# Performance work log

Hardware: AMD Instinct MI355X
Metric: run time of the kernel (lower is better)

## Reference

```python
import jax, jax.numpy as jnp
import numpy as np

N_NODES = 50000
N_EDGES = 800000
IN_CH = 256
OUT_CH = 64
HEADS = 4


def setup_inputs() -> dict:
    key = jax.random.key(0)
    k1, k2, k3, k4, k5 = jax.random.split(key, 5)
    x = jax.random.normal(k1, (N_NODES, IN_CH), dtype=jnp.float32)
    edge_index = jax.random.randint(k2, (2, N_EDGES), 0, N_NODES, dtype=jnp.int64)
    # xavier-ish scaled params
    weight = jax.random.normal(k3, (HEADS, IN_CH, OUT_CH), dtype=jnp.float32) * (2.0 / (IN_CH + OUT_CH)) ** 0.5
    att_src = jax.random.normal(k4, (1, HEADS, OUT_CH), dtype=jnp.float32) * 0.1
    att_dst = jax.random.normal(k5, (1, HEADS, OUT_CH), dtype=jnp.float32) * 0.1
    bias = jnp.zeros((HEADS * OUT_CH,), dtype=jnp.float32)
    return {"x": x, "edge_index": edge_index, "weight": weight,
            "att_src": att_src, "att_dst": att_dst, "bias": bias}


def reference(x, edge_index, weight, att_src, att_dst, bias):
    # GATConv forward (eval mode: dropout is identity), vectorized over heads.
    num_nodes = x.shape[0]
    row, col = edge_index[0], edge_index[1]
    # per-head projection: [N, H, C]
    x_h = jnp.einsum('nf,hfc->nhc', x, weight)
    alpha_src = jnp.sum(x_h * att_src[0], axis=-1)   # [N, H]
    alpha_dst = jnp.sum(x_h * att_dst[0], axis=-1)   # [N, H]
    alpha = alpha_src[row] + alpha_dst[col]          # [E, H]
    alpha = jax.nn.leaky_relu(alpha, negative_slope=0.2)
    # segment softmax over edges grouped by destination row (numerically stable)
    alpha_max = jax.ops.segment_max(alpha, row, num_segments=num_nodes)  # [N, H]
    alpha = jnp.exp(alpha - alpha_max[row])
    alpha_sum = jax.ops.segment_sum(alpha, row, num_segments=num_nodes)  # [N, H]
    alpha = alpha / jnp.clip(alpha_sum[row], 1e-16)
    # message passing: scatter-add alpha-weighted source features
    messages = alpha[:, :, None] * x_h[col]                              # [E, H, C]
    out = jax.ops.segment_sum(messages, row, num_segments=num_nodes)    # [N, H, C]
    out = out.reshape(num_nodes, -1) + bias                              # concat heads
    return out
```

## Files before the change

### kernel.cpp

```cpp
#include <hip/hip_runtime.h>
#include <hip/hip_fp16.h>
#include <math.h>

#define N_IN_CH 256
#define N_OUT   256
#define HEADS   4
#define OUT_CH  64
#define BM      64
#define SCAN_BLOCK 1024

typedef __attribute__((ext_vector_type(8))) short bf16x8;
typedef __attribute__((ext_vector_type(4))) float f32x4;

__device__ __forceinline__ float lrelu(float a) {
  return a >= 0.f ? a : 0.2f * a;
}

__device__ __forceinline__ ushort f2bf(float f) {
  uint u = __float_as_uint(f);
  uint r = (u + 0x7FFFu + ((u >> 16) & 1u)) >> 16;
  return (ushort)r;
}

__device__ __forceinline__ ushort f2h(float f) {
  return __half_as_ushort(__float2half(f));
}
__device__ __forceinline__ float h2f(ushort u) {
  return __half2float(__ushort_as_half(u));
}

__global__ void convert_w(const float* __restrict__ w, ushort* __restrict__ bt,
                          int* __restrict__ counts, int nnodes) {
  const int idx = blockIdx.x * 256 + threadIdx.x;
  if (idx < nnodes) counts[idx] = 0;
  const int n = idx >> 8, k = idx & 255;
  const int h = n >> 6, c = n & 63;
  bt[idx] = f2bf(w[h * (N_IN_CH * OUT_CH) + k * OUT_CH + c]);
}

__global__ void count_kernel(const int* __restrict__ row, int* __restrict__ counts,
                             int* __restrict__ rank, int nedges) {
  int e = blockIdx.x * blockDim.x + threadIdx.x;
  if (e < nedges) rank[e] = atomicAdd(&counts[row[e]], 1);
}

__global__ __launch_bounds__(256) void proj_mfma(
    const float* __restrict__ x, const ushort* __restrict__ bt,
    const float* __restrict__ att_src, const float* __restrict__ att_dst,
    ushort* __restrict__ xh, float* __restrict__ asrc, float* __restrict__ adst,
    int nnodes) {
  __shared__ ushort at[BM * N_IN_CH];
  const int tid = threadIdx.x;
  const int wave = tid >> 6;
  const int lane = tid & 63;
  const int n0 = blockIdx.x * BM;

  {
    const int rsub = tid >> 6;
    const int cf = (tid & 63) * 4;
    const int cb = cf * 2;
#pragma unroll
    for (int it = 0; it < 16; ++it) {
      const int row_ = it * 4 + rsub;
      const int grow = n0 + row_;
      float4 xv = make_float4(0.f, 0.f, 0.f, 0.f);
      if (grow < nnodes) xv = *(const float4*)&x[(size_t)grow * N_IN_CH + cf];
      ushort4 b;
      b.x = f2bf(xv.x); b.y = f2bf(xv.y); b.z = f2bf(xv.z); b.w = f2bf(xv.w);
      const int cbs = cb ^ ((row_ & 7) << 4);
      *(ushort4*)((char*)at + row_ * 512 + cbs) = b;
    }
  }
  __syncthreads();

  f32x4 acc[4][4];
#pragma unroll
  for (int mt = 0; mt < 4; ++mt)
#pragma unroll
    for (int nt = 0; nt < 4; ++nt) acc[mt][nt] = (f32x4){0.f, 0.f, 0.f, 0.f};

  const int lmod = lane & 15;
  const int ldiv = lane >> 4;

  for (int ks = 0; ks < 8; ++ks) {
    bf16x8 a[4], b[4];
#pragma unroll
    for (int mt = 0; mt < 4; ++mt) {
      const int row_ = mt * 16 + lmod;
      const int kb = ks * 64 + ldiv * 16;
      const int cbs = kb ^ ((row_ & 7) << 4);
      a[mt] = *(const bf16x8*)((const char*)at + row_ * 512 + cbs);
    }
#pragma unroll
    for (int nt = 0; nt < 4; ++nt) {
      const int n = wave * 64 + nt * 16 + lmod;
      b[nt] = *(const bf16x8*)&bt[(size_t)n * N_IN_CH + ks * 32 + ldiv * 8];
    }
#pragma unroll
    for (int mt = 0; mt < 4; ++mt)
#pragma unroll
      for (int nt = 0; nt < 4; ++nt)
        acc[mt][nt] = __builtin_amdgcn_mfma_f32_16x16x32_bf16(
            a[mt], b[nt], acc[mt][nt], 0, 0, 0);
  }

  float atts[4], attd[4];
#pragma unroll
  for (int nt = 0; nt < 4; ++nt) {
    const int gcol = wave * 64 + nt * 16 + lmod;
    atts[nt] = att_src[gcol];
    attd[nt] = att_dst[gcol];
  }

#pragma unroll
  for (int mt = 0; mt < 4; ++mt) {
#pragma unroll
    for (int reg = 0; reg < 4; ++reg) {
      const int grow = n0 + mt * 16 + ldiv * 4 + reg;
      const bool ok = grow < nnodes;
      float vs = 0.f, vd = 0.f;
#pragma unroll
      for (int nt = 0; nt < 4; ++nt) {
        const float v = acc[mt][nt][reg];
        if (ok) xh[(size_t)grow * N_OUT + wave * 64 + nt * 16 + lmod] = f2h(v);
        vs = fmaf(v, atts[nt], vs);
        vd = fmaf(v, attd[nt], vd);
      }
#pragma unroll
      for (int d = 1; d < 16; d <<= 1) {
        vs += __shfl_xor(vs, d, 64);
        vd += __shfl_xor(vd, d, 64);
      }
      if (lmod == 0 && ok) {
        asrc[grow * HEADS + wave] = vs;
        adst[grow * HEADS + wave] = vd;
      }
    }
  }
}

__global__ __launch_bounds__(SCAN_BLOCK) void scan1_kernel(
    const int* __restrict__ counts, int* __restrict__ offsets,
    int* __restrict__ partials, int n) {
  __shared__ int wsum[16];
  const int tid = threadIdx.x;
  const int lane = tid & 63;
  const int wid = tid >> 6;
  const int i = blockIdx.x * SCAN_BLOCK + tid;
  int v = (i < n) ? counts[i] : 0;
  int incl = v;
#pragma unroll
  for (int d = 1; d < 64; d <<= 1) {
    int t = __shfl_up(incl, d, 64);
    if (lane >= d) incl += t;
  }
  if (lane == 63) wsum[wid] = incl;
  __syncthreads();
  if (wid == 0) {
    int wv = (lane < 16) ? wsum[lane] : 0;
#pragma unroll
    for (int d = 1; d < 16; d <<= 1) {
      int t = __shfl_up(wv, d, 64);
      if (lane >= d) wv += t;
    }
    if (lane < 16) wsum[lane] = wv;
  }
  __syncthreads();
  const int wexcl = (wid == 0) ? 0 : wsum[wid - 1];
  if (i <= n) offsets[i] = wexcl + incl - v;
  if (tid == SCAN_BLOCK - 1) partials[blockIdx.x] = wsum[15];
}

__global__ void scan2_kernel(int* __restrict__ partials, int nparts) {
  const int lane = threadIdx.x;
  int v = (lane < nparts) ? partials[lane] : 0;
  int incl = v;
#pragma unroll
  for (int d = 1; d < 64; d <<= 1) {
    int t = __shfl_up(incl, d, 64);
    if (lane >= d) incl += t;
  }
  if (lane < nparts) partials[lane] = incl - v;
}

__global__ void scatter_kernel(const int* __restrict__ row, const int* __restrict__ col,
                               const int* __restrict__ rank,
                               const int* __restrict__ offsets,
                               const int* __restrict__ partials,
                               const float* __restrict__ asrc,
                               const float* __restrict__ adst,
                               uint4* __restrict__ erec, int nedges) {
  int e = blockIdx.x * blockDim.x + threadIdx.x;
  if (e < nedges) {
    const int r = row[e];
    const int c = col[e];
    const int pos = offsets[r] + partials[r >> 10] + rank[e];
    const float4 s = *(const float4*)&asrc[r * 4];
    const float4 d = *(const float4*)&adst[c * 4];
    uint4 rec;
    rec.x = (uint)c;
    rec.y = (uint)f2h(__expf(lrelu(s.x + d.x))) |
            ((uint)f2h(__expf(lrelu(s.y + d.y))) << 16);
    rec.z = (uint)f2h(__expf(lrelu(s.z + d.z))) |
            ((uint)f2h(__expf(lrelu(s.w + d.w))) << 16);
    rec.w = 0u;
    erec[pos] = rec;
  }
}

__global__ __launch_bounds__(256) void gather_kernel(
    const int* __restrict__ offsets, const int* __restrict__ partials,
    const uint4* __restrict__ erec,
    const ushort* __restrict__ xh, const float* __restrict__ bias,
    float* __restrict__ out, int nnodes) {
  __shared__ float pbuf[4][64 * 4];
  const int wv = threadIdx.x >> 6;
  const int lane = threadIdx.x & 63;
  const int n = blockIdx.x * 4 + wv;
  if (n >= nnodes) return;
  const int off = offsets[n] + partials[n >> 10];
  const int end = offsets[n + 1] + partials[(n + 1) >> 10];
  const int deg = end - off;
  const int half = lane >> 5;
  const int ch8 = (lane & 31) * 8;
  const int hh = (lane & 31) >> 3;

  float4 s4 = make_float4(0.f, 0.f, 0.f, 0.f);
  float a0 = 0.f, a1 = 0.f, a2 = 0.f, a3 = 0.f;
  float a4 = 0.f, a5 = 0.f, a6 = 0.f, a7 = 0.f;

  for (int b = 0; b < deg; b += 64) {
    const int cnt = min(64, deg - b);
    int cl_l = 0;
    float4 p = make_float4(0.f, 0.f, 0.f, 0.f);
    if (lane < cnt) {
      const uint4 rec = erec[off + b + lane];
      cl_l = (int)rec.x;
      p.x = h2f((ushort)(rec.y & 0xFFFFu));
      p.y = h2f((ushort)(rec.y >> 16));
      p.z = h2f((ushort)(rec.z & 0xFFFFu));
      p.w = h2f((ushort)(rec.z >> 16));
      s4.x += p.x; s4.y += p.y; s4.z += p.z; s4.w += p.w;
    }
    *(float4*)&pbuf[wv][lane * 4] = p;

    for (int j = 0; j < cnt; j += 16) {
      int cq[8];
#pragma unroll
      for (int q = 0; q < 8; ++q) cq[q] = __shfl(cl_l, j + 2 * q + half, 64);
      uint4 xq[8];
#pragma unroll
      for (int q = 0; q < 8; ++q)
        xq[q] = *(const uint4*)&xh[(size_t)cq[q] * N_OUT + ch8];

      float wq[8];
#pragma unroll
      for (int q = 0; q < 8; ++q) wq[q] = pbuf[wv][(j + 2 * q + half) * 4 + hh];

#pragma unroll
      for (int q = 0; q < 8; ++q) {
        a0 = fmaf(wq[q], h2f((ushort)(xq[q].x & 0xFFFFu)), a0);
        a1 = fmaf(wq[q], h2f((ushort)(xq[q].x >> 16)), a1);
        a2 = fmaf(wq[q], h2f((ushort)(xq[q].y & 0xFFFFu)), a2);
        a3 = fmaf(wq[q], h2f((ushort)(xq[q].y >> 16)), a3);
        a4 = fmaf(wq[q], h2f((ushort)(xq[q].z & 0xFFFFu)), a4);
        a5 = fmaf(wq[q], h2f((ushort)(xq[q].z >> 16)), a5);
        a6 = fmaf(wq[q], h2f((ushort)(xq[q].w & 0xFFFFu)), a6);
        a7 = fmaf(wq[q], h2f((ushort)(xq[q].w >> 16)), a7);
      }
    }
  }

  a0 += __shfl_xor(a0, 32, 64);
  a1 += __shfl_xor(a1, 32, 64);
  a2 += __shfl_xor(a2, 32, 64);
  a3 += __shfl_xor(a3, 32, 64);
  a4 += __shfl_xor(a4, 32, 64);
  a5 += __shfl_xor(a5, 32, 64);
  a6 += __shfl_xor(a6, 32, 64);
  a7 += __shfl_xor(a7, 32, 64);

#pragma unroll
  for (int d = 1; d < 64; d <<= 1) {
    s4.x += __shfl_xor(s4.x, d, 64);
    s4.y += __shfl_xor(s4.y, d, 64);
    s4.z += __shfl_xor(s4.z, d, 64);
    s4.w += __shfl_xor(s4.w, d, 64);
  }
  const float sh = (hh == 0) ? s4.x : (hh == 1) ? s4.y : (hh == 2) ? s4.z : s4.w;
  const float invh = 1.f / fmaxf(sh, 1e-16f);

  const int wch = ch8 + half * 4;
  const float4 b4 = *(const float4*)&bias[wch];
  float4 o;
  o.x = fmaf(half ? a4 : a0, invh, b4.x);
  o.y = fmaf(half ? a5 : a1, invh, b4.y);
  o.z = fmaf(half ? a6 : a2, invh, b4.z);
  o.w = fmaf(half ? a7 : a3, invh, b4.w);
  *(float4*)&out[(size_t)n * N_OUT + wch] = o;
}

extern "C" void kernel_launch(void* const* d_in, const int* in_sizes, int n_in,
                              void* d_out, int out_size, void* d_ws, size_t ws_size,
                              hipStream_t stream) {
  const float* x        = (const float*)d_in[0];
  const int*   edge_idx = (const int*)d_in[1];
  const float* weight   = (const float*)d_in[2];
  const float* att_src  = (const float*)d_in[3];
  const float* att_dst  = (const float*)d_in[4];
  const float* bias     = (const float*)d_in[5];
  float* out = (float*)d_out;

  const int nnodes = in_sizes[0] / N_IN_CH;
  const int nedges = in_sizes[1] / 2;
  const int* row = edge_idx;
  const int* col = edge_idx + nedges;

  char* wsb = (char*)d_ws;
  size_t woff = 0;
  auto alloc = [&](size_t bytes) -> char* {
    char* p = wsb + woff;
    woff += (bytes + 255) & ~(size_t)255;
    return p;
  };
  ushort* xh    = (ushort*)alloc((size_t)nnodes * N_OUT * sizeof(ushort));
  ushort* bt    = (ushort*)alloc((size_t)N_OUT * N_IN_CH * sizeof(ushort));
  float* asrc   = (float*)alloc((size_t)nnodes * HEADS * sizeof(float));
  float* adst   = (float*)alloc((size_t)nnodes * HEADS * sizeof(float));
  int* counts   = (int*)alloc((size_t)nnodes * sizeof(int));
  int* offsets  = (int*)alloc((size_t)(nnodes + 1) * sizeof(int));
  int* partials = (int*)alloc(256 * sizeof(int));
  int* rank     = (int*)alloc((size_t)nedges * sizeof(int));
  uint4* erec   = (uint4*)alloc((size_t)nedges * sizeof(uint4));

  convert_w<<<256, 256, 0, stream>>>(weight, bt, counts, nnodes);

  const int eblocks = (nedges + 255) / 256;
  count_kernel<<<eblocks, 256, 0, stream>>>(row, counts, rank, nedges);

  const int nblocksA = (nnodes + BM - 1) / BM;
  proj_mfma<<<nblocksA, 256, 0, stream>>>(x, bt, att_src, att_dst,
                                          xh, asrc, adst, nnodes);

  const int nscan = (nnodes + 1 + SCAN_BLOCK - 1) / SCAN_BLOCK;
  scan1_kernel<<<nscan, SCAN_BLOCK, 0, stream>>>(counts, offsets, partials, nnodes);
  scan2_kernel<<<1, 64, 0, stream>>>(partials, nscan);

  scatter_kernel<<<eblocks, 256, 0, stream>>>(row, col, rank, offsets, partials,
                                              asrc, adst, erec, nedges);

  gather_kernel<<<(nnodes + 3) / 4, 256, 0, stream>>>(offsets, partials, erec,
                                                      xh, bias, out, nnodes);
}
```

Measured before the change: 168.2 us.

## Fuse edge counting into projection launch and inline partial-sum scan

Merges the edge-count atomic kernel into the projection kernel as extra blocks, so counting edges can run alongside the MFMA projection in one launch. Removes the single-wave second-level scan kernel; each wave in scatter and gather now recomputes the exclusive scan of block partials and fetches its value with a cross-lane shuffle. This saves two kernel launches and their serialization gaps. In exchange it adds redundant per-wave scan work and shares the projection's large static LDS allocation with the count blocks, which may limit occupancy.

Result: faster. 160.7 us (-4.4%).

```diff
diff --git a/kernel.cpp b/kernel.cpp
--- a/kernel.cpp
+++ b/kernel.cpp
@@ -27,6 +27,18 @@
 }
 __device__ __forceinline__ float h2f(ushort u) {
   return __half2float(__ushort_as_half(u));
+}
+
+__device__ __forceinline__ int wave_scan_partials(const int* __restrict__ partials,
+                                                  int nparts, int lane) {
+  int pv = (lane < nparts) ? partials[lane] : 0;
+  int incl = pv;
+#pragma unroll
+  for (int d = 1; d < 64; d <<= 1) {
+    int t = __shfl_up(incl, d, 64);
+    if (lane >= d) incl += t;
+  }
+  return incl - pv;
 }
 
 __global__ void convert_w(const float* __restrict__ w, ushort* __restrict__ bt,
@@ -38,19 +50,22 @@
   bt[idx] = f2bf(w[h * (N_IN_CH * OUT_CH) + k * OUT_CH + c]);
 }
 
-__global__ void count_kernel(const int* __restrict__ row, int* __restrict__ counts,
-                             int* __restrict__ rank, int nedges) {
-  int e = blockIdx.x * blockDim.x + threadIdx.x;
-  if (e < nedges) rank[e] = atomicAdd(&counts[row[e]], 1);
-}
-
-__global__ __launch_bounds__(256) void proj_mfma(
+__global__ __launch_bounds__(256) void proj_count(
     const float* __restrict__ x, const ushort* __restrict__ bt,
     const float* __restrict__ att_src, const float* __restrict__ att_dst,
     ushort* __restrict__ xh, float* __restrict__ asrc, float* __restrict__ adst,
-    int nnodes) {
+    int nnodes, int nblocksA,
+    const int* __restrict__ row, int* __restrict__ counts,
+    int* __restrict__ rank, int nedges) {
   __shared__ ushort at[BM * N_IN_CH];
   const int tid = threadIdx.x;
+
+  if (blockIdx.x >= nblocksA) {
+    const int e = (blockIdx.x - nblocksA) * 256 + tid;
+    if (e < nedges) rank[e] = atomicAdd(&counts[row[e]], 1);
+    return;
+  }
+
   const int wave = tid >> 6;
   const int lane = tid & 63;
   const int n0 = blockIdx.x * BM;
@@ -171,30 +186,20 @@
   if (tid == SCAN_BLOCK - 1) partials[blockIdx.x] = wsum[15];
 }
 
-__global__ void scan2_kernel(int* __restrict__ partials, int nparts) {
-  const int lane = threadIdx.x;
-  int v = (lane < nparts) ? partials[lane] : 0;
-  int incl = v;
-#pragma unroll
-  for (int d = 1; d < 64; d <<= 1) {
-    int t = __shfl_up(incl, d, 64);
-    if (lane >= d) incl += t;
-  }
-  if (lane < nparts) partials[lane] = incl - v;
-}
-
 __global__ void scatter_kernel(const int* __restrict__ row, const int* __restrict__ col,
                                const int* __restrict__ rank,
                                const int* __restrict__ offsets,
-                               const int* __restrict__ partials,
+                               const int* __restrict__ partials, int nparts,
                                const float* __restrict__ asrc,
                                const float* __restrict__ adst,
                                uint4* __restrict__ erec, int nedges) {
+  const int lane = threadIdx.x & 63;
+  const int excl = wave_scan_partials(partials, nparts, lane);
   int e = blockIdx.x * blockDim.x + threadIdx.x;
   if (e < nedges) {
     const int r = row[e];
     const int c = col[e];
-    const int pos = offsets[r] + partials[r >> 10] + rank[e];
+    const int pos = offsets[r] + __shfl(excl, r >> 10, 64) + rank[e];
     const float4 s = *(const float4*)&asrc[r * 4];
     const float4 d = *(const float4*)&adst[c * 4];
     uint4 rec;
@@ -209,7 +214,8 @@
 }
 
 __global__ __launch_bounds__(256) void gather_kernel(
-    const int* __restrict__ offsets, const int* __restrict__ partials,
+    const int* __restrict__ offsets,
+    const int* __restrict__ partials, int nparts,
     const uint4* __restrict__ erec,
     const ushort* __restrict__ xh, const float* __restrict__ bias,
     float* __restrict__ out, int nnodes) {
@@ -218,8 +224,9 @@
   const int lane = threadIdx.x & 63;
   const int n = blockIdx.x * 4 + wv;
   if (n >= nnodes) return;
-  const int off = offsets[n] + partials[n >> 10];
-  const int end = offsets[n + 1] + partials[(n + 1) >> 10];
+  const int excl = wave_scan_partials(partials, nparts, lane);
+  const int off = offsets[n] + __shfl(excl, n >> 10, 64);
+  const int end = offsets[n + 1] + __shfl(excl, (n + 1) >> 10, 64);
   const int deg = end - off;
   const int half = lane >> 5;
   const int ch8 = (lane & 31) * 8;
@@ -336,19 +343,18 @@
   convert_w<<<256, 256, 0, stream>>>(weight, bt, counts, nnodes);
 
   const int eblocks = (nedges + 255) / 256;
-  count_kernel<<<eblocks, 256, 0, stream>>>(row, counts, rank, nedges);
-
   const int nblocksA = (nnodes + BM - 1) / BM;
-  proj_mfma<<<nblocksA, 256, 0, stream>>>(x, bt, att_src, att_dst,
-                                          xh, asrc, adst, nnodes);
+  proj_count<<<nblocksA + eblocks, 256, 0, stream>>>(
+      x, bt, att_src, att_dst, xh, asrc, adst, nnodes, nblocksA,
+      row, counts, rank, nedges);
 
   const int nscan = (nnodes + 1 + SCAN_BLOCK - 1) / SCAN_BLOCK;
   scan1_kernel<<<nscan, SCAN_BLOCK, 0, stream>>>(counts, offsets, partials, nnodes);
-  scan2_kernel<<<1, 64, 0, stream>>>(partials, nscan);
-
-  scatter_kernel<<<eblocks, 256, 0, stream>>>(row, col, rank, offsets, partials,
+
+  scatter_kernel<<<eblocks, 256, 0, stream>>>(row, col, rank, offsets,
+                                              partials, nscan,
                                               asrc, adst, erec, nedges);
 
-  gather_kernel<<<(nnodes + 3) / 4, 256, 0, stream>>>(offsets, partials, erec,
-                                                      xh, bias, out, nnodes);
-}
+  gather_kernel<<<(nnodes + 3) / 4, 256, 0, stream>>>(offsets, partials, nscan,
+                                                      erec, xh, bias, out, nnodes);
+}
```
